# Performance work log

Measured on AMD Instinct MI355X. Metric: run time of the kernel, lower is better.

## Reference

```python
import jax, jax.numpy as jnp
import numpy as np

B, T, I, H = 1024, 2048, 12, 512


def setup_inputs() -> dict:
    key = jax.random.key(0)
    k1, k2, k3, k4 = jax.random.split(key, 4)
    s = 1.0 / np.sqrt(H)
    return {
        "history": jax.random.normal(k1, (B, T, I), dtype=jnp.float32),
        "w_ih": jax.random.normal(k2, (3 * H, I), dtype=jnp.float32) * s,
        "w_hh": jax.random.normal(k3, (3 * H, H), dtype=jnp.float32) * s,
        "w_out": jax.random.normal(k4, (2, H), dtype=jnp.float32) * s,
        "b_out": jnp.zeros((2,), dtype=jnp.float32),
    }


def reference(history, w_ih, w_hh, w_out, b_out):
    # GRUCell recurrence over T steps with per-step linear head (torch GRUCell math, bias=False)
    xs = jnp.transpose(history, (1, 0, 2))  # [T, B, I]
    h0 = jnp.zeros((history.shape[0], H), dtype=history.dtype)

    def step(h, x_t):
        gi = x_t @ w_ih.T            # [B, 3H]
        gh = h @ w_hh.T              # [B, 3H]
        i_r, i_z, i_n = jnp.split(gi, 3, axis=-1)
        h_r, h_z, h_n = jnp.split(gh, 3, axis=-1)
        r = jax.nn.sigmoid(i_r + h_r)
        z = jax.nn.sigmoid(i_z + h_z)
        n = jnp.tanh(i_n + r * h_n)
        h_new = (1.0 - z) * n + z * h
        logit = h_new @ w_out.T + b_out  # [B, 2]
        return h_new, logit

    h_final, logits = jax.lax.scan(step, h0, xs)
    return jnp.transpose(logits, (1, 0, 2)), h_final  # ([B, T, 2], [B, H])
```

## Files before the change

### kernel.cpp

```cpp
#include <hip/hip_runtime.h>
#include <stdint.h>


#define NB 256
#define NT 256
#define TB 1024
#define TT 2048
#define II 12
#define HH 512
#define NCL 32
#define GBLK 8
#define ROWS 32

#define HTILE_B (ROWS * HH * 2)
#define HBUF_B  ((size_t)NCL * HTILE_B)
#define BAR_OFF ((size_t)2 * HBUF_B)
#define WS_USED (BAR_OFF + NCL * 128)

#define LDSB (ROWS * 1024)

#define GAS __attribute__((address_space(1)))
#define LAS __attribute__((address_space(3)))

typedef _Float16 half8 __attribute__((ext_vector_type(8)));
typedef float    f32x4 __attribute__((ext_vector_type(4)));

static __device__ __forceinline__ float fast_sigmoid(float x) {
  float e = exp2f(-1.44269504f * x);
  return __builtin_amdgcn_rcpf(1.0f + e);
}
static __device__ __forceinline__ float fast_tanh(float x) {
  float e = exp2f(2.88539008f * x);
  return 1.0f - 2.0f * __builtin_amdgcn_rcpf(1.0f + e);
}

static __device__ __forceinline__ void wait_flags8(unsigned* f, unsigned tgt,
                                                   int* dead) {
  const int l = threadIdx.x & 63;
  long spin = 0;
  for (;;) {
    unsigned v = __hip_atomic_load(f + (l & 7), __ATOMIC_RELAXED,
                                   __HIP_MEMORY_SCOPE_AGENT);
    if (__all(v >= tgt)) break;
    if (++spin > (1L << 24)) { *dead = 1; break; }
  }
}

__global__ void __launch_bounds__(NT, 1)
gru_persistent(const float* __restrict__ hist,
               const float* __restrict__ w_ih,
               const float* __restrict__ w_hh,
               const float* __restrict__ w_out,
               const float* __restrict__ b_out,
               float* __restrict__ out,
               uint8_t* __restrict__ ws)
{
  extern __shared__ char smem[];
  char* ldsA = smem;
  const int bid = blockIdx.x;
  const int c   = bid & 31;
  const int g   = bid >> 5;
  const int tid = threadIdx.x;
  const int w   = tid >> 6;
  const int l   = tid & 63;
  const int l15 = l & 15;
  const int l4  = l >> 4;
  const int crb = c * ROWS;
  unsigned* flags = (unsigned*)(ws + BAR_OFF) + c * 32;

  const int col0 = g * 64 + w * 16;

  half8 wr[16], wz[16], wn[16];
#pragma unroll
  for (int ks = 0; ks < 16; ++ks) {
    const size_t Rr = (size_t)(0 * HH + col0 + l15) * HH + ks * 32 + l4 * 8;
    const size_t Rz = (size_t)(1 * HH + col0 + l15) * HH + ks * 32 + l4 * 8;
    const size_t Rn = (size_t)(2 * HH + col0 + l15) * HH + ks * 32 + l4 * 8;
#pragma unroll
    for (int i = 0; i < 8; ++i) {
      wr[ks][i] = (_Float16)w_hh[Rr + i];
      wz[ks][i] = (_Float16)w_hh[Rz + i];
      wn[ks][i] = (_Float16)w_hh[Rn + i];
    }
  }

  half8 wih[3];
#pragma unroll
  for (int gt = 0; gt < 3; ++gt) {
    const int R = gt * HH + col0 + l15;
#pragma unroll
    for (int i = 0; i < 8; ++i) {
      const int k = l4 * 8 + i;
      wih[gt][i] = (_Float16)((k < II) ? w_ih[R * II + k] : 0.0f);
    }
  }

  const int jj = (l >> 4) & 1;
  float wor[32];
#pragma unroll
  for (int i = 0; i < 32; ++i) wor[i] = w_out[jj * HH + l15 * 32 + i];
  const float bo = b_out[jj];

  float hprev[2][4];
#pragma unroll
  for (int mt = 0; mt < 2; ++mt)
#pragma unroll
    for (int q = 0; q < 4; ++q) hprev[mt][q] = 0.0f;

  const int pcol = col0 + l15;
  int deadlock = 0;

  f32x4 xn0[2], xn1[2];
#pragma unroll
  for (int mt = 0; mt < 2; ++mt) {
    xn0[mt] = (f32x4){0.f, 0.f, 0.f, 0.f};
    xn1[mt] = (f32x4){0.f, 0.f, 0.f, 0.f};
    const float* xp = hist + (size_t)(crb + mt * 16 + l15) * (TT * II);
    if (l4 == 0)      { xn0[mt] = *(const f32x4*)xp; xn1[mt] = *(const f32x4*)(xp + 4); }
    else if (l4 == 1) { xn0[mt] = *(const f32x4*)(xp + 8); }
  }

  for (int t = 0; t < TT; ++t) {
    const uint8_t* hsrc = ws + ((t & 1) ? HBUF_B : 0) + (size_t)c * HTILE_B;
    uint8_t*       hdst = ws + ((t & 1) ? 0 : HBUF_B) + (size_t)c * HTILE_B;

    if (t > 0) wait_flags8(flags, (unsigned)t, &deadlock);

#pragma unroll
    for (int it = 0; it < 8; ++it)
      __builtin_amdgcn_global_load_lds(
          (const GAS uint32_t*)(hsrc + it * 4096 + tid * 16),
          (LAS uint32_t*)(ldsA + it * 4096 + tid * 16), 16, 0, 17);
    __builtin_amdgcn_sched_barrier(0);

    half8 ax[2];
#pragma unroll
    for (int mt = 0; mt < 2; ++mt)
#pragma unroll
      for (int i = 0; i < 4; ++i) {
        ax[mt][i]     = (_Float16)xn0[mt][i];
        ax[mt][4 + i] = (_Float16)xn1[mt][i];
      }
    {
      const int tx = (t + 1 < TT) ? (t + 1) : 0;
#pragma unroll
      for (int mt = 0; mt < 2; ++mt) {
        const float* xp = hist + (size_t)(crb + mt * 16 + l15) * (TT * II) + (size_t)tx * II;
        if (l4 == 0)      { xn0[mt] = *(const f32x4*)xp; xn1[mt] = *(const f32x4*)(xp + 4); }
        else if (l4 == 1) { xn0[mt] = *(const f32x4*)(xp + 8); }
      }
    }
    __builtin_amdgcn_sched_barrier(0);

    asm volatile("s_waitcnt vmcnt(10)" ::: "memory");
    __builtin_amdgcn_s_barrier();
    __builtin_amdgcn_sched_barrier(0);

    f32x4 acc0, acc1, acc2, accin;

    acc0 = (f32x4){0.f, 0.f, 0.f, 0.f};
    acc1 = acc0; acc2 = acc0;
    accin = __builtin_amdgcn_mfma_f32_16x16x32_f16(ax[0], wih[2],
              (f32x4){0.f, 0.f, 0.f, 0.f}, 0, 0, 0);
    acc0 = __builtin_amdgcn_mfma_f32_16x16x32_f16(ax[0], wih[0], acc0, 0, 0, 0);
    acc1 = __builtin_amdgcn_mfma_f32_16x16x32_f16(ax[0], wih[1], acc1, 0, 0, 0);
#pragma unroll
    for (int ks = 0; ks < 16; ++ks) {
      const int ko = (ks * 64 + l4 * 16) ^ ((l15 & 7) << 4);
      half8 a = *(const half8*)(ldsA + l15 * 1024 + ko);
      acc0 = __builtin_amdgcn_mfma_f32_16x16x32_f16(a, wr[ks], acc0, 0, 0, 0);
      acc1 = __builtin_amdgcn_mfma_f32_16x16x32_f16(a, wz[ks], acc1, 0, 0, 0);
      acc2 = __builtin_amdgcn_mfma_f32_16x16x32_f16(a, wn[ks], acc2, 0, 0, 0);
    }
#pragma unroll
    for (int q = 0; q < 4; ++q) {
      const int m = l4 * 4 + q;
      const float r  = fast_sigmoid(acc0[q]);
      const float z  = fast_sigmoid(acc1[q]);
      const float n  = fast_tanh(accin[q] + r * acc2[q]);
      const float hn = (1.0f - z) * n + z * hprev[0][q];
      hprev[0][q] = hn;
      const unsigned short hu = __builtin_bit_cast(unsigned short, (_Float16)hn);
      __hip_atomic_store(
          (unsigned short*)(hdst + m * 1024 + ((pcol * 2) ^ ((m & 7) << 4))),
          hu, __ATOMIC_RELAXED, __HIP_MEMORY_SCOPE_AGENT);
    }
    __builtin_amdgcn_sched_barrier(0);

    asm volatile("s_waitcnt vmcnt(10)" ::: "memory");
    __builtin_amdgcn_s_barrier();
    __builtin_amdgcn_sched_barrier(0);

    acc0 = (f32x4){0.f, 0.f, 0.f, 0.f};
    acc1 = acc0; acc2 = acc0;
    accin = __builtin_amdgcn_mfma_f32_16x16x32_f16(ax[1], wih[2],
              (f32x4){0.f, 0.f, 0.f, 0.f}, 0, 0, 0);
    acc0 = __builtin_amdgcn_mfma_f32_16x16x32_f16(ax[1], wih[0], acc0, 0, 0, 0);
    acc1 = __builtin_amdgcn_mfma_f32_16x16x32_f16(ax[1], wih[1], acc1, 0, 0, 0);
#pragma unroll
    for (int ks = 0; ks < 16; ++ks) {
      const int ko = (ks * 64 + l4 * 16) ^ ((l15 & 7) << 4);
      half8 a = *(const half8*)(ldsA + (16 + l15) * 1024 + ko);
      acc0 = __builtin_amdgcn_mfma_f32_16x16x32_f16(a, wr[ks], acc0, 0, 0, 0);
      acc1 = __builtin_amdgcn_mfma_f32_16x16x32_f16(a, wz[ks], acc1, 0, 0, 0);
      acc2 = __builtin_amdgcn_mfma_f32_16x16x32_f16(a, wn[ks], acc2, 0, 0, 0);
    }
#pragma unroll
    for (int q = 0; q < 4; ++q) {
      const int m = 16 + l4 * 4 + q;
      const float r  = fast_sigmoid(acc0[q]);
      const float z  = fast_sigmoid(acc1[q]);
      const float n  = fast_tanh(accin[q] + r * acc2[q]);
      const float hn = (1.0f - z) * n + z * hprev[1][q];
      hprev[1][q] = hn;
      const unsigned short hu = __builtin_bit_cast(unsigned short, (_Float16)hn);
      __hip_atomic_store(
          (unsigned short*)(hdst + m * 1024 + ((pcol * 2) ^ ((m & 7) << 4))),
          hu, __ATOMIC_RELAXED, __HIP_MEMORY_SCOPE_AGENT);
    }

    if (t > 0) {
      const int lr  = ((g * 4 + w) & 31);
      const int row = crb + lr;
      float s = 0.0f;
#pragma unroll
      for (int c8 = 0; c8 < 4; ++c8) {
        half8 hv = *(const half8*)(ldsA + lr * 1024 +
                                   ((l15 * 64 + c8 * 16) ^ ((lr & 7) << 4)));
#pragma unroll
        for (int i = 0; i < 8; ++i) s += (float)hv[i] * wor[c8 * 8 + i];
      }
#pragma unroll
      for (int off = 1; off < 16; off <<= 1) s += __shfl_xor(s, off);
      if (l15 == 0 && l < 32) out[((size_t)row * TT + (t - 1)) * 2 + jj] = s + bo;
    }

    asm volatile("s_waitcnt vmcnt(0)" ::: "memory");
    __builtin_amdgcn_s_barrier();
    if (tid == 0)
      __hip_atomic_store(flags + g, (unsigned)(t + 1), __ATOMIC_RELAXED,
                         __HIP_MEMORY_SCOPE_AGENT);
  }

  wait_flags8(flags, (unsigned)TT, &deadlock);
  {
    const uint8_t* hsrc = ws + ((TT & 1) ? HBUF_B : 0) + (size_t)c * HTILE_B;
#pragma unroll
    for (int it = 0; it < 8; ++it)
      __builtin_amdgcn_global_load_lds(
          (const GAS uint32_t*)(hsrc + it * 4096 + tid * 16),
          (LAS uint32_t*)(ldsA + it * 4096 + tid * 16), 16, 0, 17);
    asm volatile("s_waitcnt vmcnt(0)" ::: "memory");
    __builtin_amdgcn_s_barrier();

    const int lr  = ((g * 4 + w) & 31);
    const int row = crb + lr;
    float s = 0.0f;
#pragma unroll
    for (int c8 = 0; c8 < 4; ++c8) {
      half8 hv = *(const half8*)(ldsA + lr * 1024 +
                                 ((l15 * 64 + c8 * 16) ^ ((lr & 7) << 4)));
#pragma unroll
      for (int i = 0; i < 8; ++i) s += (float)hv[i] * wor[c8 * 8 + i];
    }
#pragma unroll
    for (int off = 1; off < 16; off <<= 1) s += __shfl_xor(s, off);
    if (l15 == 0 && l < 32) out[((size_t)row * TT + (TT - 1)) * 2 + jj] = s + bo;
  }

#pragma unroll
  for (int mt = 0; mt < 2; ++mt)
#pragma unroll
    for (int q = 0; q < 4; ++q) {
      const int m = mt * 16 + l4 * 4 + q;
      out[(size_t)TB * TT * 2 + (size_t)(crb + m) * HH + pcol] = hprev[mt][q];
    }
}

extern "C" void kernel_launch(void* const* d_in, const int* in_sizes, int n_in,
                              void* d_out, int out_size, void* d_ws, size_t ws_size,
                              hipStream_t stream) {
  (void)in_sizes; (void)n_in; (void)out_size;
  if (ws_size < WS_USED) return;

  const float* hist  = (const float*)d_in[0];
  const float* w_ih  = (const float*)d_in[1];
  const float* w_hh  = (const float*)d_in[2];
  const float* w_out = (const float*)d_in[3];
  const float* b_out = (const float*)d_in[4];
  float* out = (float*)d_out;
  uint8_t* ws = (uint8_t*)d_ws;

  hipMemsetAsync(d_ws, 0, WS_USED, stream);

  void* args[] = {(void*)&hist, (void*)&w_ih, (void*)&w_hh, (void*)&w_out,
                  (void*)&b_out, (void*)&out, (void*)&ws};
  hipError_t e = hipLaunchCooperativeKernel((const void*)gru_persistent,
                                            dim3(NB), dim3(NT), args,
                                            (unsigned)LDSB, stream);
  if (e != hipSuccess) {
    gru_persistent<<<dim3(NB), dim3(NT), LDSB, stream>>>(
        hist, w_ih, w_hh, w_out, b_out, out, ws);
  }
}
```

Measured before the change: 7.627 ms.

## Split per-step barrier into per-wave half-tile flags to overlap row halves

Replaces the single per-block step flag with per-wave flags, kept separately for the low and high 16-row halves of the hidden-state tile. A consumer now waits only for the first half before loading it, and fetches the second half after computing the first. Flag values are prefetched so the spin loop is skipped when producers are already done. The aim is to shorten the grid-wide barrier critical path by pipelining the two half-tiles, at the cost of more flag traffic and tighter ordering requirements between stores and flag updates.

```diff
diff --git a/kernel.cpp b/kernel.cpp
--- a/kernel.cpp
+++ b/kernel.cpp
@@ -15,7 +15,7 @@
 #define HTILE_B (ROWS * HH * 2)
 #define HBUF_B  ((size_t)NCL * HTILE_B)
 #define BAR_OFF ((size_t)2 * HBUF_B)
-#define WS_USED (BAR_OFF + NCL * 128)
+#define WS_USED (BAR_OFF + (size_t)NCL * 256)
 
 #define LDSB (ROWS * 1024)
 
@@ -34,12 +34,12 @@
   return 1.0f - 2.0f * __builtin_amdgcn_rcpf(1.0f + e);
 }
 
-static __device__ __forceinline__ void wait_flags8(unsigned* f, unsigned tgt,
-                                                   int* dead) {
+static __device__ __forceinline__ void wait_flags32(unsigned* f, unsigned tgt,
+                                                    int* dead) {
   const int l = threadIdx.x & 63;
   long spin = 0;
   for (;;) {
-    unsigned v = __hip_atomic_load(f + (l & 7), __ATOMIC_RELAXED,
+    unsigned v = __hip_atomic_load(f + (l & 31), __ATOMIC_RELAXED,
                                    __HIP_MEMORY_SCOPE_AGENT);
     if (__all(v >= tgt)) break;
     if (++spin > (1L << 24)) { *dead = 1; break; }
@@ -66,7 +66,9 @@
   const int l15 = l & 15;
   const int l4  = l >> 4;
   const int crb = c * ROWS;
-  unsigned* flags = (unsigned*)(ws + BAR_OFF) + c * 32;
+  unsigned* loF = (unsigned*)(ws + BAR_OFF) + (size_t)c * 64;
+  unsigned* hiF = loF + 32;
+  const int myflag = g * 4 + w;
 
   const int col0 = g * 64 + w * 16;
 
@@ -120,14 +122,17 @@
     else if (l4 == 1) { xn0[mt] = *(const f32x4*)(xp + 8); }
   }
 
+  unsigned preLo = 0, preHi = 0;
+
   for (int t = 0; t < TT; ++t) {
     const uint8_t* hsrc = ws + ((t & 1) ? HBUF_B : 0) + (size_t)c * HTILE_B;
     uint8_t*       hdst = ws + ((t & 1) ? 0 : HBUF_B) + (size_t)c * HTILE_B;
 
-    if (t > 0) wait_flags8(flags, (unsigned)t, &deadlock);
-
-#pragma unroll
-    for (int it = 0; it < 8; ++it)
+    if (!__all(preLo >= (unsigned)t)) wait_flags32(loF, (unsigned)t, &deadlock);
+    __builtin_amdgcn_sched_barrier(0);
+
+#pragma unroll
+    for (int it = 0; it < 4; ++it)
       __builtin_amdgcn_global_load_lds(
           (const GAS uint32_t*)(hsrc + it * 4096 + tid * 16),
           (LAS uint32_t*)(ldsA + it * 4096 + tid * 16), 16, 0, 17);
@@ -150,18 +155,18 @@
         else if (l4 == 1) { xn0[mt] = *(const f32x4*)(xp + 8); }
       }
     }
-    __builtin_amdgcn_sched_barrier(0);
-
-    asm volatile("s_waitcnt vmcnt(10)" ::: "memory");
+    preHi = __hip_atomic_load(hiF + (l & 31), __ATOMIC_RELAXED,
+                              __HIP_MEMORY_SCOPE_AGENT);
+    __builtin_amdgcn_sched_barrier(0);
+
+    asm volatile("s_waitcnt vmcnt(7)" ::: "memory");
     __builtin_amdgcn_s_barrier();
     __builtin_amdgcn_sched_barrier(0);
 
-    f32x4 acc0, acc1, acc2, accin;
-
-    acc0 = (f32x4){0.f, 0.f, 0.f, 0.f};
-    acc1 = acc0; acc2 = acc0;
-    accin = __builtin_amdgcn_mfma_f32_16x16x32_f16(ax[0], wih[2],
-              (f32x4){0.f, 0.f, 0.f, 0.f}, 0, 0, 0);
+    f32x4 acc0 = (f32x4){0.f, 0.f, 0.f, 0.f};
+    f32x4 acc1 = acc0, acc2 = acc0;
+    f32x4 accin = __builtin_amdgcn_mfma_f32_16x16x32_f16(ax[0], wih[2],
+                    (f32x4){0.f, 0.f, 0.f, 0.f}, 0, 0, 0);
     acc0 = __builtin_amdgcn_mfma_f32_16x16x32_f16(ax[0], wih[0], acc0, 0, 0, 0);
     acc1 = __builtin_amdgcn_mfma_f32_16x16x32_f16(ax[0], wih[1], acc1, 0, 0, 0);
 #pragma unroll
@@ -172,6 +177,16 @@
       acc1 = __builtin_amdgcn_mfma_f32_16x16x32_f16(a, wz[ks], acc1, 0, 0, 0);
       acc2 = __builtin_amdgcn_mfma_f32_16x16x32_f16(a, wn[ks], acc2, 0, 0, 0);
     }
+
+    if (!__all(preHi >= (unsigned)t)) wait_flags32(hiF, (unsigned)t, &deadlock);
+    __builtin_amdgcn_sched_barrier(0);
+#pragma unroll
+    for (int it = 0; it < 4; ++it)
+      __builtin_amdgcn_global_load_lds(
+          (const GAS uint32_t*)(hsrc + 16384 + it * 4096 + tid * 16),
+          (LAS uint32_t*)(ldsA + 16384 + it * 4096 + tid * 16), 16, 0, 17);
+    __builtin_amdgcn_sched_barrier(0);
+
 #pragma unroll
     for (int q = 0; q < 4; ++q) {
       const int m = l4 * 4 + q;
@@ -187,7 +202,10 @@
     }
     __builtin_amdgcn_sched_barrier(0);
 
-    asm volatile("s_waitcnt vmcnt(10)" ::: "memory");
+    asm volatile("s_waitcnt vmcnt(0)" ::: "memory");
+    if (l == 0)
+      __hip_atomic_store(loF + myflag, (unsigned)(t + 1), __ATOMIC_RELAXED,
+                         __HIP_MEMORY_SCOPE_AGENT);
     __builtin_amdgcn_s_barrier();
     __builtin_amdgcn_sched_barrier(0);
 
@@ -220,7 +238,7 @@
     }
 
     if (t > 0) {
-      const int lr  = ((g * 4 + w) & 31);
+      const int lr  = g * 4 + w;
       const int row = crb + lr;
       float s = 0.0f;
 #pragma unroll
@@ -236,13 +254,15 @@
     }
 
     asm volatile("s_waitcnt vmcnt(0)" ::: "memory");
-    __builtin_amdgcn_s_barrier();
-    if (tid == 0)
-      __hip_atomic_store(flags + g, (unsigned)(t + 1), __ATOMIC_RELAXED,
+    if (l == 0)
+      __hip_atomic_store(hiF + myflag, (unsigned)(t + 1), __ATOMIC_RELAXED,
                          __HIP_MEMORY_SCOPE_AGENT);
-  }
-
-  wait_flags8(flags, (unsigned)TT, &deadlock);
+    preLo = __hip_atomic_load(loF + (l & 31), __ATOMIC_RELAXED,
+                              __HIP_MEMORY_SCOPE_AGENT);
+  }
+
+  wait_flags32(loF, (unsigned)TT, &deadlock);
+  wait_flags32(hiF, (unsigned)TT, &deadlock);
   {
     const uint8_t* hsrc = ws + ((TT & 1) ? HBUF_B : 0) + (size_t)c * HTILE_B;
 #pragma unroll
@@ -253,7 +273,7 @@
     asm volatile("s_waitcnt vmcnt(0)" ::: "memory");
     __builtin_amdgcn_s_barrier();
 
-    const int lr  = ((g * 4 + w) & 31);
+    const int lr  = g * 4 + w;
     const int row = crb + lr;
     float s = 0.0f;
 #pragma unroll
```

Measured after the change: 8.727 ms. +14.4%, slower.
